# Optimization experiments

Measured on AMD Instinct MI355X. Metric: run time of the kernel, lower is better.

Reference implementation:

```python
import jax, jax.numpy as jnp
import numpy as np

B_SZ, L, H, P, G, N, CS = 2, 2048, 32, 64, 1, 128, 256


def _i8(k, shape):
    return jax.random.randint(k, shape, -127, 128, dtype=jnp.int32).astype(jnp.int8)


def setup_inputs() -> dict:
    key = jax.random.key(0)
    k = jax.random.split(key, 7)
    return {
        "x": _i8(k[0], (B_SZ, L, H, P)),          # quantized int8 activations
        "dt": _i8(k[1], (B_SZ, L, H)),
        "B": _i8(k[2], (B_SZ, L, G, N)),
        "C": _i8(k[3], (B_SZ, L, G, N)),
        "q_A_log": _i8(k[4], (H,)),               # int8 quantized A_log
        "q_D": _i8(k[5], (H,)),                   # int8 quantized D (D_has_hdim=False)
        "dt_bias": jax.random.normal(k[6], (H,), jnp.float32) * 0.1,
        "A_log_scale": jnp.float32(0.02),
        "D_scale": jnp.float32(0.01),
        "dt_scale": jnp.float32(0.03),
        "x_scale": jnp.float32(0.05),
        "B_scale": jnp.float32(0.05),
        "C_scale": jnp.float32(0.05),
    }


def _chunk_scan(x, dt, B, C, q_A_log, q_D, dt_bias,
                A_log_scale, D_scale, dt_scale, x_scale, B_scale, C_scale):
    f32 = jnp.float32
    b, l, h, p = x.shape
    g, n = B.shape[2], B.shape[3]
    cs = CS
    nc = l // cs

    # --- inline dequantization (per-tensor scales, nhead/ndim groups == 0) ---
    xf = x.astype(f32) * x_scale                       # (b, l, h, p)
    dtf = jax.nn.softplus(dt.astype(f32) * dt_scale + dt_bias)   # (b, l, h), dt_limit=(0, inf)
    A = -jnp.exp(q_A_log.astype(f32) * A_log_scale)    # (h,)
    Bf = B.astype(f32) * B_scale                       # (b, l, g, n)
    Cf = C.astype(f32) * C_scale

    # --- chunk the sequence ---
    xc = xf.reshape(b, nc, cs, h, p)
    dtc = dtf.reshape(b, nc, cs, h)
    Bc = Bf.reshape(b, nc, cs, g, n)
    Cc = Cf.reshape(b, nc, cs, g, n)
    rep = h // g
    Bh = jnp.repeat(Bc, rep, axis=3)                   # (b, nc, cs, h, n)
    Ch = jnp.repeat(Cc, rep, axis=3)

    dA = dtc * A                                       # (b, nc, cs, h), <= 0
    cum = jnp.cumsum(dA, axis=2)                       # cumulative log-decay within chunk

    # --- per-chunk states: sum_s exp(cum[-1]-cum[s]) * dt[s] * B[s] (x) x[s] ---
    decay_states = jnp.exp(cum[:, :, -1:, :] - cum)    # (b, nc, cs, h)
    states = jnp.einsum('bzlhn,bzlh,bzlhp->bzhpn', Bh, dtc * decay_states, xc)

    # --- inter-chunk recurrence (sequential scan over chunks) ---
    chunk_decay = jnp.exp(cum[:, :, -1, :])            # (b, nc, h)

    def step(carry, inp):
        s_c, d_c = inp                                 # (b, h, p, n), (b, h)
        new = d_c[:, :, None, None] * carry + s_c
        return new, carry                              # emit state entering this chunk

    states_t = jnp.moveaxis(states, 1, 0)              # (nc, b, h, p, n)
    decay_t = jnp.moveaxis(chunk_decay, 1, 0)          # (nc, b, h)
    final_state, prev_states = jax.lax.scan(
        step, jnp.zeros((b, h, p, n), f32), (states_t, decay_t))
    prev_states = jnp.moveaxis(prev_states, 0, 1)      # (b, nc, h, p, n)

    # --- inter-chunk output: C[l] . state_in * exp(cum[l]) ---
    y_inter = jnp.einsum('bzlhn,bzhpn,bzlh->bzlhp', Ch, prev_states, jnp.exp(cum))

    # --- intra-chunk output: causal (C.B) attention with decay weights ---
    cumT = jnp.moveaxis(cum, 3, 2)                     # (b, nc, h, cs)
    diff = cumT[..., :, None] - cumT[..., None, :]     # (b, nc, h, cs, cs): cum[l]-cum[s]
    mask = jnp.tril(jnp.ones((cs, cs), bool))
    decay_m = jnp.exp(jnp.where(mask, diff, -jnp.inf)) # zero above diagonal, no overflow
    scores = (jnp.einsum('bzlhn,bzshn->bzhls', Ch, Bh)
              * decay_m
              * jnp.moveaxis(dtc, 3, 2)[..., None, :])
    y_intra = jnp.einsum('bzhls,bzshp->bzlhp', scores, xc)

    # --- skip connection D * x (per-head D) ---
    Df = q_D.astype(f32) * D_scale                     # (h,)
    y = (y_intra + y_inter).reshape(b, l, h, p) + xf * Df[None, None, :, None]
    return y


def reference(x, dt, B, C, q_A_log, q_D, dt_bias,
              A_log_scale, D_scale, dt_scale, x_scale, B_scale, C_scale):
    return _chunk_scan(x, dt, B, C, q_A_log, q_D, dt_bias,
                       A_log_scale, D_scale, dt_scale, x_scale, B_scale, C_scale)
```

## Files before the change

kernel.cpp:

```cpp
#include <hip/hip_runtime.h>
#include <math.h>

#define BB 2
#define LSEQ 2048
#define H 32
#define PDIM 64
#define NDIM 128
#define CS 256
#define NC 8

typedef _Float16 half8 __attribute__((ext_vector_type(8)));
typedef float floatx4 __attribute__((ext_vector_type(4)));


__device__ __forceinline__ int dot4i8(int a, int b, int c) {
#if __has_builtin(__builtin_amdgcn_sdot4)
    return __builtin_amdgcn_sdot4(a, b, c, false);
#else
    c += ((a << 24) >> 24) * ((b << 24) >> 24);
    c += ((a << 16) >> 24) * ((b << 16) >> 24);
    c += ((a << 8) >> 24) * ((b << 8) >> 24);
    c += (a >> 24) * (b >> 24);
    return c;
#endif
}

__global__ __launch_bounds__(256) void k1_dtcum(
    const int* __restrict__ dt, const int* __restrict__ qA,
    const float* __restrict__ dt_bias,
    const float* __restrict__ A_scale_p, const float* __restrict__ dt_scale_p,
    float* __restrict__ dtf, float* __restrict__ cum, float* __restrict__ cdecay)
{
    int t = threadIdx.x;
    int h = blockIdx.x & 31;
    int z = (blockIdx.x >> 5) & 7;
    int b = blockIdx.x >> 8;
    int l = z * CS + t;
    float dt_scale = *dt_scale_p;
    float A = -__expf((float)qA[h] * (*A_scale_p));
    float raw = (float)dt[(b * LSEQ + l) * H + h];
    float xin = raw * dt_scale + dt_bias[h];
    float sp = (xin > 20.f) ? xin : log1pf(__expf(xin));
    float dA = sp * A;

    __shared__ float arr[CS];
    arr[t] = dA;
    __syncthreads();
    for (int off = 1; off < CS; off <<= 1) {
        float v = (t >= off) ? arr[t - off] : 0.f;
        __syncthreads();
        arr[t] += v;
        __syncthreads();
    }
    int base = ((b * NC + z) * H + h) * CS;
    dtf[base + t] = sp;
    cum[base + t] = arr[t];
    if (t == CS - 1) cdecay[(b * NC + z) * H + h] = __expf(arr[t]);
}

__global__ __launch_bounds__(256) void k2_cb(
    const int* __restrict__ Bm, const int* __restrict__ Cm,
    const float* __restrict__ Bs_p, const float* __restrict__ Cs_p,
    float* __restrict__ CBt)
{
    __shared__ int Bi[64][33];
    __shared__ int Ci[64][33];
    const int LT[10] = {0,1,1,2,2,2,3,3,3,3};
    const int ST[10] = {0,0,1,0,1,2,0,1,2,3};
    int t = threadIdx.x;
    int tile = blockIdx.x % 10;
    int zz = blockIdx.x / 10;
    int z = zz & 7, b = zz >> 3;
    int bz = b * NC + z;
    int l0 = LT[tile] * 64, s0 = ST[tile] * 64;
    const int* Bp = Bm + (size_t)(b * LSEQ + z * CS + s0) * NDIM;
    const int* Cp = Cm + (size_t)(b * LSEQ + z * CS + l0) * NDIM;
    for (int i = t; i < 64 * 32; i += 256) {
        int r = i >> 5, k = i & 31;
        const int* sb = Bp + r * NDIM + k * 4;
        const int* sc = Cp + r * NDIM + k * 4;
        Bi[r][k] = (sb[0] & 255) | ((sb[1] & 255) << 8) | ((sb[2] & 255) << 16) | ((sb[3] & 255) << 24);
        Ci[r][k] = (sc[0] & 255) | ((sc[1] & 255) << 8) | ((sc[2] & 255) << 16) | ((sc[3] & 255) << 24);
    }
    __syncthreads();
    float cbscale = (*Bs_p) * (*Cs_p);
    int ll = t & 63, lg = t >> 6;
    int acc[16];
#pragma unroll
    for (int i = 0; i < 16; ++i) acc[i] = 0;
    for (int k = 0; k < 32; ++k) {
        int cw = Ci[ll][k];
#pragma unroll
        for (int si = 0; si < 16; ++si)
            acc[si] = dot4i8(cw, Bi[lg * 16 + si][k], acc[si]);
    }
    int l = l0 + ll;
    int l16 = l >> 4, lm = l & 15;
    int sb8 = (s0 + lg * 16) >> 3;
    float* bp = CBt + ((size_t)(bz * 16 + l16) * 32 + sb8) * 128 + lm * 8;
#pragma unroll
    for (int g = 0; g < 2; ++g) {
        floatx4 v0, v1;
#pragma unroll
        for (int i = 0; i < 4; ++i) {
            v0[i] = (float)acc[g * 8 + i] * cbscale;
            v1[i] = (float)acc[g * 8 + 4 + i] * cbscale;
        }
        *(floatx4*)(bp + g * 128) = v0;
        *(floatx4*)(bp + g * 128 + 4) = v1;
    }
}

__global__ __launch_bounds__(256) void kprep(
    const int* __restrict__ Bm, const int* __restrict__ Cm,
    _Float16* __restrict__ Bt16T, _Float16* __restrict__ C16T)
{
    int t = threadIdx.x;
    int slice = blockIdx.x & 15, z = (blockIdx.x >> 4) & 7, b = blockIdx.x >> 7;
    int bz = b * NC + z;
    {
        int lm = t >> 4, n8 = t & 15;
        const int* cp = Cm + (size_t)(b * LSEQ + z * CS + slice * 16 + lm) * NDIM + n8 * 8;
        int4 c0 = *(const int4*)cp;
        int4 c1 = *(const int4*)(cp + 4);
        half8 v;
        v[0] = (_Float16)(float)c0.x; v[1] = (_Float16)(float)c0.y;
        v[2] = (_Float16)(float)c0.z; v[3] = (_Float16)(float)c0.w;
        v[4] = (_Float16)(float)c1.x; v[5] = (_Float16)(float)c1.y;
        v[6] = (_Float16)(float)c1.z; v[7] = (_Float16)(float)c1.w;
        *(half8*)(C16T + ((size_t)(bz * 16 + slice) * 16 + n8) * 128 + lm * 8) = v;
    }
    {
        int nm = t & 15, s8l = t >> 4;
        int n16 = slice & 7, s8 = (slice >> 3) * 16 + s8l;
        const int* bp = Bm + (size_t)(b * LSEQ + z * CS + s8 * 8) * NDIM + n16 * 16 + nm;
        half8 v;
#pragma unroll
        for (int j = 0; j < 8; ++j) v[j] = (_Float16)(float)bp[(size_t)j * NDIM];
        *(half8*)(Bt16T + ((size_t)(bz * 8 + n16) * 32 + s8) * 128 + nm * 8) = v;
    }
}

__global__ __launch_bounds__(256) void k0x(
    const int* __restrict__ xq, const float* __restrict__ dtf, const float* __restrict__ cum,
    const float* __restrict__ xs_p, const float* __restrict__ Bs_p,
    _Float16* __restrict__ xTdtT, _Float16* __restrict__ xTcT)
{
    __shared__ float cA[CS], cB[CS];
    int t = threadIdx.x;
    int h = blockIdx.x & 31, z = (blockIdx.x >> 5) & 7, b = blockIdx.x >> 8;
    int bzh = ((b * NC + z) * H + h);
    int base = bzh * CS;
    float xs = *xs_p, Bs = *Bs_p;
    {
        float d = dtf[base + t], c = cum[base + t], cl = cum[base + CS - 1];
        cA[t] = d * xs;
        cB[t] = d * __expf(cl - c) * xs * Bs;
    }
    __syncthreads();
    int s8 = t & 31, pg = t >> 5;
    const int* xb = xq + ((size_t)(b * LSEQ + z * CS) * H + h) * PDIM + pg * 8;
    half8 va[8], vc[8];
#pragma unroll
    for (int j = 0; j < 8; ++j) {
        int s = s8 * 8 + j;
        const int* xp = xb + (size_t)s * (H * PDIM);
        int4 lo = *(const int4*)xp;
        int4 hi = *(const int4*)(xp + 4);
        float a = cA[s], c = cB[s];
#define CVT(PL, V) { float xv = (float)(V); va[PL][j] = (_Float16)(xv * a); vc[PL][j] = (_Float16)(xv * c); }
        CVT(0, lo.x) CVT(1, lo.y) CVT(2, lo.z) CVT(3, lo.w)
        CVT(4, hi.x) CVT(5, hi.y) CVT(6, hi.z) CVT(7, hi.w)
#undef CVT
    }
    int p16 = pg >> 1;
#pragma unroll
    for (int pl = 0; pl < 8; ++pl) {
        int p = pg * 8 + pl;
        size_t off = ((size_t)(bzh * 4 + p16) * 32 + s8) * 128 + (p & 15) * 8;
        *(half8*)(xTdtT + off) = va[pl];
        *(half8*)(xTcT + off) = vc[pl];
    }
}

__global__ __launch_bounds__(256) void k3m(
    const _Float16* __restrict__ xTcT, const _Float16* __restrict__ Bt16T,
    const float* __restrict__ cum, float* __restrict__ states)
{
    __shared__ float cume[8];
    int t = threadIdx.x;
    int h = blockIdx.x & 31, z = (blockIdx.x >> 5) & 7, b = blockIdx.x >> 8;
    int bz = b * NC + z, bzh = bz * H + h;
    if (t < 8) cume[t] = cum[bzh * CS + t * 32 + 31];
    __syncthreads();
    float cl = cume[7];
    int w = t >> 6, lane = t & 63, m = lane & 15, q = lane >> 4;
    const _Float16* abase = xTcT + ((size_t)(bzh * 4 + w) * 32) * 128 + m * 8;
    const _Float16* bbase = Bt16T + (size_t)(bz * 8) * 32 * 128 + m * 8;
    floatx4 acc[8] = {};
    for (int kk = 0; kk < 8; ++kk) {
        if (cl - cume[kk] < -30.f) continue;
        int s8 = kk * 4 + q;
        half8 a = *(const half8*)(abase + (size_t)s8 * 128);
#pragma unroll
        for (int nt = 0; nt < 8; ++nt) {
            half8 bf = *(const half8*)(bbase + ((size_t)nt * 32 + s8) * 128);
            acc[nt] = __builtin_amdgcn_mfma_f32_16x16x32_f16(a, bf, acc[nt], 0, 0, 0);
        }
    }
    float* sb = states + (size_t)bzh * (PDIM * NDIM);
#pragma unroll
    for (int nt = 0; nt < 8; ++nt)
#pragma unroll
        for (int r = 0; r < 4; ++r)
            sb[(size_t)(w * 16 + q * 4 + r) * NDIM + nt * 16 + m] = acc[nt][r];
}

__global__ __launch_bounds__(256) void k4_scan(
    const float* __restrict__ cdecay, const float* __restrict__ states,
    _Float16* __restrict__ statesHT)
{
    int idx = blockIdx.x * 256 + threadIdx.x;
    int i = idx & 8191, h = (idx >> 13) & 31, b = idx >> 18;
    int p = i >> 7, n = i & 127;
    int toff = ((p >> 4) * 16 + (n >> 3)) * 128 + (p & 15) * 8 + (n & 7);
    float carry = 0.f;
    for (int z = 0; z < NC; ++z) {
        int bzh = (b * NC + z) * H + h;
        float v = states[(size_t)bzh * 8192 + i];
        float d = cdecay[bzh];
        statesHT[(size_t)bzh * 8192 + toff] = (_Float16)(carry * 0.0625f);
        carry = d * carry + v;
    }
}

__global__ __launch_bounds__(256) void k56(
    const int* __restrict__ xq, const int* __restrict__ qD,
    const float* __restrict__ cum, const float* __restrict__ CBt,
    const _Float16* __restrict__ xTdtT, const _Float16* __restrict__ C16T,
    const _Float16* __restrict__ statesHT,
    const float* __restrict__ Cs_p, const float* __restrict__ xs_p, const float* __restrict__ Ds_p,
    float* __restrict__ out)
{
    __shared__ float cumL[CS];
    __shared__ float ep[128][65];
    int t = threadIdx.x;
    int h = blockIdx.x & 31, z = (blockIdx.x >> 5) & 7, b = blockIdx.x >> 8;
    int bz = b * NC + z, bzh = bz * H + h;
    cumL[t] = cum[bzh * CS + t];
    __syncthreads();
    int w = t >> 6, lane = t & 63, m = lane & 15, q = lane >> 4;
    floatx4 acc[4][4] = {};

    const _Float16* shb = statesHT + (size_t)bzh * 8192 + m * 8;
    const _Float16* cbase = C16T + (size_t)bz * 16 * 16 * 128 + m * 8;
    bool interact[4];
#pragma unroll
    for (int j = 0; j < 4; ++j) interact[j] = (cumL[(4 * j + w) * 16] > -80.f);
    for (int kk = 0; kk < 4; ++kk) {
        int n8 = kk * 4 + q;
        half8 bf[4];
#pragma unroll
        for (int pt = 0; pt < 4; ++pt)
            bf[pt] = *(const half8*)(shb + (pt * 16 + n8) * 128);
#pragma unroll
        for (int j = 0; j < 4; ++j) {
            if (!interact[j]) continue;
            half8 ha = *(const half8*)(cbase + ((size_t)(4 * j + w) * 16 + n8) * 128);
#pragma unroll
            for (int pt = 0; pt < 4; ++pt)
                acc[j][pt] = __builtin_amdgcn_mfma_f32_16x16x32_f16(ha, bf[pt], acc[j][pt], 0, 0, 0);
        }
    }
    float Cs16 = (*Cs_p) * 16.0f;
#pragma unroll
    for (int j = 0; j < 4; ++j)
#pragma unroll
        for (int r = 0; r < 4; ++r) {
            float e = __expf(cumL[(4 * j + w) * 16 + q * 4 + r]) * Cs16;
#pragma unroll
            for (int pt = 0; pt < 4; ++pt) acc[j][pt][r] *= e;
        }

    const float* cbtb = CBt + (size_t)bz * 16 * 32 * 128 + m * 8;
    const _Float16* xb = xTdtT + (size_t)bzh * 4 * 32 * 128 + m * 8;
    for (int kk = 0; kk < 8; ++kk) {
        int jmin = (2 * kk - w + 3) >> 2;
        if (jmin < 0) jmin = 0;
        if (jmin > 3) continue;
        int s8 = kk * 4 + q;
        half8 bf[4];
#pragma unroll
        for (int pt = 0; pt < 4; ++pt)
            bf[pt] = *(const half8*)(xb + ((size_t)pt * 32 + s8) * 128);
        float cs_hi = cumL[kk * 32 + 31];
#pragma unroll
        for (int j = 0; j < 4; ++j) {
            if (j < jmin) continue;
            int l16 = 4 * j + w;
            if (cumL[l16 * 16] - cs_hi < -30.f) continue;
            int lA = l16 * 16 + m;
            float cum_l = cumL[lA];
            const float* cp = cbtb + ((size_t)l16 * 32 + s8) * 128;
            floatx4 c0 = *(const floatx4*)cp;
            floatx4 c1 = *(const floatx4*)(cp + 4);
            half8 a;
#pragma unroll
            for (int jj = 0; jj < 8; ++jj) {
                int s = kk * 32 + q * 8 + jj;
                float cb = (jj < 4) ? c0[jj] : c1[jj - 4];
                float wv = cb * __expf(cum_l - cumL[s]);
                a[jj] = (_Float16)((s <= lA) ? wv : 0.f);
            }
#pragma unroll
            for (int pt = 0; pt < 4; ++pt)
                acc[j][pt] = __builtin_amdgcn_mfma_f32_16x16x32_f16(a, bf[pt], acc[j][pt], 0, 0, 0);
        }
    }

    float xsDf = (*xs_p) * ((float)qD[h] * (*Ds_p));
    __syncthreads();
#pragma unroll
    for (int pass = 0; pass < 2; ++pass) {
#pragma unroll
        for (int jj = 0; jj < 2; ++jj) {
            int j = pass * 2 + jj;
            int lbase = (((4 * j + w) * 16) & 127) + q * 4;
#pragma unroll
            for (int r = 0; r < 4; ++r)
#pragma unroll
                for (int pt = 0; pt < 4; ++pt)
                    ep[lbase + r][pt * 16 + m] = acc[j][pt][r];
        }
        __syncthreads();
        int lloc = t >> 1;
        int l = pass * 128 + lloc;
        size_t go = ((size_t)(b * LSEQ + z * CS + l) * H + h) * PDIM + (t & 1) * 32;
        const float* er = &ep[lloc][(t & 1) * 32];
#pragma unroll
        for (int it = 0; it < 8; ++it) {
            int4 xv = *(const int4*)(xq + go + it * 4);
            floatx4 v;
            v[0] = er[it * 4 + 0] + (float)xv.x * xsDf;
            v[1] = er[it * 4 + 1] + (float)xv.y * xsDf;
            v[2] = er[it * 4 + 2] + (float)xv.z * xsDf;
            v[3] = er[it * 4 + 3] + (float)xv.w * xsDf;
            *(floatx4*)(out + go + it * 4) = v;
        }
        __syncthreads();
    }
}

extern "C" void kernel_launch(void* const* d_in, const int* in_sizes, int n_in,
                              void* d_out, int out_size, void* d_ws, size_t ws_size,
                              hipStream_t stream)
{
    const int* xq = (const int*)d_in[0];
    const int* dt = (const int*)d_in[1];
    const int* Bm = (const int*)d_in[2];
    const int* Cm = (const int*)d_in[3];
    const int* qA = (const int*)d_in[4];
    const int* qD = (const int*)d_in[5];
    const float* dt_bias = (const float*)d_in[6];
    const float* A_scale = (const float*)d_in[7];
    const float* D_scale = (const float*)d_in[8];
    const float* dt_scale = (const float*)d_in[9];
    const float* x_scale = (const float*)d_in[10];
    const float* B_scale = (const float*)d_in[11];
    const float* C_scale = (const float*)d_in[12];
    float* out = (float*)d_out;

    char* ws = (char*)d_ws;
    float* dtf          = (float*)(ws);
    float* cum          = (float*)(ws + 524288);
    float* cdecay       = (float*)(ws + 1048576);
    float* CBt          = (float*)(ws + 1052672);
    float* states       = (float*)(ws + 5246976);
    _Float16* xTdtT     = (_Float16*)(ws + 22024192);
    _Float16* xTcT      = (_Float16*)(ws + 38801408);
    _Float16* statesHT  = (_Float16*)(ws + 38801408);
    _Float16* Bt16T     = (_Float16*)(ws + 55578624);
    _Float16* C16T      = (_Float16*)(ws + 56627200);

    k1_dtcum<<<dim3(512), dim3(256), 0, stream>>>(dt, qA, dt_bias, A_scale, dt_scale,
                                                  dtf, cum, cdecay);
    k2_cb<<<dim3(160), dim3(256), 0, stream>>>(Bm, Cm, B_scale, C_scale, CBt);
    kprep<<<dim3(256), dim3(256), 0, stream>>>(Bm, Cm, Bt16T, C16T);
    k0x<<<dim3(512), dim3(256), 0, stream>>>(xq, dtf, cum, x_scale, B_scale, xTdtT, xTcT);
    k3m<<<dim3(512), dim3(256), 0, stream>>>(xTcT, Bt16T, cum, states);
    k4_scan<<<dim3(2048), dim3(256), 0, stream>>>(cdecay, states, statesHT);
    k56<<<dim3(512), dim3(256), 0, stream>>>(xq, qD, cum, CBt, xTdtT, C16T, statesHT,
                                             C_scale, x_scale, D_scale, out);
}
```

Before: 177.0 us.

## Fuse prep kernels, compute chunk states from LDS, compact x to int8

Merges the CB-score and B/C fp16 prep kernels into one launch. A second fused kernel does the dt softplus, the cumulative sum via wavefront shuffles, the x conversion and the state MFMA, keeping the decayed x tile in LDS instead of going through a global buffer. It also writes an int8 copy of x so the final kernel reads a quarter of the bytes for the skip term, and the scan kernel now processes four elements per thread. This cuts launches and global round-trips, at the cost of more LDS and register use in the fused kernel and an extra int8 write.

```diff
diff --git a/kernel.cpp b/kernel.cpp
--- a/kernel.cpp
+++ b/kernel.cpp
@@ -10,6 +10,7 @@
 #define NC 8
 
 typedef _Float16 half8 __attribute__((ext_vector_type(8)));
+typedef _Float16 half4 __attribute__((ext_vector_type(4)));
 typedef float floatx4 __attribute__((ext_vector_type(4)));
 
 
@@ -25,186 +26,174 @@
 #endif
 }
 
-__global__ __launch_bounds__(256) void k1_dtcum(
-    const int* __restrict__ dt, const int* __restrict__ qA,
-    const float* __restrict__ dt_bias,
-    const float* __restrict__ A_scale_p, const float* __restrict__ dt_scale_p,
-    float* __restrict__ dtf, float* __restrict__ cum, float* __restrict__ cdecay)
-{
-    int t = threadIdx.x;
-    int h = blockIdx.x & 31;
-    int z = (blockIdx.x >> 5) & 7;
-    int b = blockIdx.x >> 8;
-    int l = z * CS + t;
-    float dt_scale = *dt_scale_p;
-    float A = -__expf((float)qA[h] * (*A_scale_p));
-    float raw = (float)dt[(b * LSEQ + l) * H + h];
-    float xin = raw * dt_scale + dt_bias[h];
-    float sp = (xin > 20.f) ? xin : log1pf(__expf(xin));
-    float dA = sp * A;
-
-    __shared__ float arr[CS];
-    arr[t] = dA;
-    __syncthreads();
-    for (int off = 1; off < CS; off <<= 1) {
-        float v = (t >= off) ? arr[t - off] : 0.f;
-        __syncthreads();
-        arr[t] += v;
-        __syncthreads();
-    }
-    int base = ((b * NC + z) * H + h) * CS;
-    dtf[base + t] = sp;
-    cum[base + t] = arr[t];
-    if (t == CS - 1) cdecay[(b * NC + z) * H + h] = __expf(arr[t]);
-}
-
-__global__ __launch_bounds__(256) void k2_cb(
+__global__ __launch_bounds__(256) void kA(
     const int* __restrict__ Bm, const int* __restrict__ Cm,
     const float* __restrict__ Bs_p, const float* __restrict__ Cs_p,
-    float* __restrict__ CBt)
+    float* __restrict__ CBt, _Float16* __restrict__ Bt16T, _Float16* __restrict__ C16T)
 {
     __shared__ int Bi[64][33];
     __shared__ int Ci[64][33];
-    const int LT[10] = {0,1,1,2,2,2,3,3,3,3};
-    const int ST[10] = {0,0,1,0,1,2,0,1,2,3};
     int t = threadIdx.x;
-    int tile = blockIdx.x % 10;
-    int zz = blockIdx.x / 10;
+    int r = blockIdx.x % 26;
+    int zz = blockIdx.x / 26;
     int z = zz & 7, b = zz >> 3;
     int bz = b * NC + z;
-    int l0 = LT[tile] * 64, s0 = ST[tile] * 64;
-    const int* Bp = Bm + (size_t)(b * LSEQ + z * CS + s0) * NDIM;
-    const int* Cp = Cm + (size_t)(b * LSEQ + z * CS + l0) * NDIM;
-    for (int i = t; i < 64 * 32; i += 256) {
-        int r = i >> 5, k = i & 31;
-        const int* sb = Bp + r * NDIM + k * 4;
-        const int* sc = Cp + r * NDIM + k * 4;
-        Bi[r][k] = (sb[0] & 255) | ((sb[1] & 255) << 8) | ((sb[2] & 255) << 16) | ((sb[3] & 255) << 24);
-        Ci[r][k] = (sc[0] & 255) | ((sc[1] & 255) << 8) | ((sc[2] & 255) << 16) | ((sc[3] & 255) << 24);
-    }
-    __syncthreads();
-    float cbscale = (*Bs_p) * (*Cs_p);
-    int ll = t & 63, lg = t >> 6;
-    int acc[16];
-#pragma unroll
-    for (int i = 0; i < 16; ++i) acc[i] = 0;
-    for (int k = 0; k < 32; ++k) {
-        int cw = Ci[ll][k];
-#pragma unroll
-        for (int si = 0; si < 16; ++si)
-            acc[si] = dot4i8(cw, Bi[lg * 16 + si][k], acc[si]);
-    }
-    int l = l0 + ll;
-    int l16 = l >> 4, lm = l & 15;
-    int sb8 = (s0 + lg * 16) >> 3;
-    float* bp = CBt + ((size_t)(bz * 16 + l16) * 32 + sb8) * 128 + lm * 8;
-#pragma unroll
-    for (int g = 0; g < 2; ++g) {
-        floatx4 v0, v1;
-#pragma unroll
-        for (int i = 0; i < 4; ++i) {
-            v0[i] = (float)acc[g * 8 + i] * cbscale;
-            v1[i] = (float)acc[g * 8 + 4 + i] * cbscale;
-        }
-        *(floatx4*)(bp + g * 128) = v0;
-        *(floatx4*)(bp + g * 128 + 4) = v1;
-    }
-}
-
-__global__ __launch_bounds__(256) void kprep(
-    const int* __restrict__ Bm, const int* __restrict__ Cm,
-    _Float16* __restrict__ Bt16T, _Float16* __restrict__ C16T)
-{
-    int t = threadIdx.x;
-    int slice = blockIdx.x & 15, z = (blockIdx.x >> 4) & 7, b = blockIdx.x >> 7;
-    int bz = b * NC + z;
-    {
-        int lm = t >> 4, n8 = t & 15;
-        const int* cp = Cm + (size_t)(b * LSEQ + z * CS + slice * 16 + lm) * NDIM + n8 * 8;
-        int4 c0 = *(const int4*)cp;
-        int4 c1 = *(const int4*)(cp + 4);
-        half8 v;
-        v[0] = (_Float16)(float)c0.x; v[1] = (_Float16)(float)c0.y;
-        v[2] = (_Float16)(float)c0.z; v[3] = (_Float16)(float)c0.w;
-        v[4] = (_Float16)(float)c1.x; v[5] = (_Float16)(float)c1.y;
-        v[6] = (_Float16)(float)c1.z; v[7] = (_Float16)(float)c1.w;
-        *(half8*)(C16T + ((size_t)(bz * 16 + slice) * 16 + n8) * 128 + lm * 8) = v;
-    }
-    {
-        int nm = t & 15, s8l = t >> 4;
-        int n16 = slice & 7, s8 = (slice >> 3) * 16 + s8l;
-        const int* bp = Bm + (size_t)(b * LSEQ + z * CS + s8 * 8) * NDIM + n16 * 16 + nm;
-        half8 v;
-#pragma unroll
-        for (int j = 0; j < 8; ++j) v[j] = (_Float16)(float)bp[(size_t)j * NDIM];
-        *(half8*)(Bt16T + ((size_t)(bz * 8 + n16) * 32 + s8) * 128 + nm * 8) = v;
-    }
-}
-
-__global__ __launch_bounds__(256) void k0x(
-    const int* __restrict__ xq, const float* __restrict__ dtf, const float* __restrict__ cum,
-    const float* __restrict__ xs_p, const float* __restrict__ Bs_p,
-    _Float16* __restrict__ xTdtT, _Float16* __restrict__ xTcT)
-{
+    if (r < 10) {
+        const int LT[10] = {0,1,1,2,2,2,3,3,3,3};
+        const int ST[10] = {0,0,1,0,1,2,0,1,2,3};
+        int l0 = LT[r] * 64, s0 = ST[r] * 64;
+        const int* Bp = Bm + (size_t)(b * LSEQ + z * CS + s0) * NDIM;
+        const int* Cp = Cm + (size_t)(b * LSEQ + z * CS + l0) * NDIM;
+        for (int i = t; i < 64 * 32; i += 256) {
+            int rr = i >> 5, k = i & 31;
+            const int* sb = Bp + rr * NDIM + k * 4;
+            const int* sc = Cp + rr * NDIM + k * 4;
+            Bi[rr][k] = (sb[0] & 255) | ((sb[1] & 255) << 8) | ((sb[2] & 255) << 16) | ((sb[3] & 255) << 24);
+            Ci[rr][k] = (sc[0] & 255) | ((sc[1] & 255) << 8) | ((sc[2] & 255) << 16) | ((sc[3] & 255) << 24);
+        }
+        __syncthreads();
+        float cbscale = (*Bs_p) * (*Cs_p);
+        int ll = t & 63, lg = t >> 6;
+        int acc[16];
+#pragma unroll
+        for (int i = 0; i < 16; ++i) acc[i] = 0;
+        for (int k = 0; k < 32; ++k) {
+            int cw = Ci[ll][k];
+#pragma unroll
+            for (int si = 0; si < 16; ++si)
+                acc[si] = dot4i8(cw, Bi[lg * 16 + si][k], acc[si]);
+        }
+        int l = l0 + ll;
+        int l16 = l >> 4, lm = l & 15;
+        int sb8 = (s0 + lg * 16) >> 3;
+        float* bp = CBt + ((size_t)(bz * 16 + l16) * 32 + sb8) * 128 + lm * 8;
+#pragma unroll
+        for (int g = 0; g < 2; ++g) {
+            floatx4 v0, v1;
+#pragma unroll
+            for (int i = 0; i < 4; ++i) {
+                v0[i] = (float)acc[g * 8 + i] * cbscale;
+                v1[i] = (float)acc[g * 8 + 4 + i] * cbscale;
+            }
+            *(floatx4*)(bp + g * 128) = v0;
+            *(floatx4*)(bp + g * 128 + 4) = v1;
+        }
+    } else {
+        int slice = r - 10;
+        {
+            int lm = t >> 4, n8 = t & 15;
+            const int* cp = Cm + (size_t)(b * LSEQ + z * CS + slice * 16 + lm) * NDIM + n8 * 8;
+            int4 c0 = *(const int4*)cp;
+            int4 c1 = *(const int4*)(cp + 4);
+            half8 v;
+            v[0] = (_Float16)(float)c0.x; v[1] = (_Float16)(float)c0.y;
+            v[2] = (_Float16)(float)c0.z; v[3] = (_Float16)(float)c0.w;
+            v[4] = (_Float16)(float)c1.x; v[5] = (_Float16)(float)c1.y;
+            v[6] = (_Float16)(float)c1.z; v[7] = (_Float16)(float)c1.w;
+            *(half8*)(C16T + ((size_t)(bz * 16 + slice) * 16 + n8) * 128 + lm * 8) = v;
+        }
+        {
+            int nm = t & 15, s8l = t >> 4;
+            int n16 = slice & 7, s8 = (slice >> 3) * 16 + s8l;
+            const int* bp = Bm + (size_t)(b * LSEQ + z * CS + s8 * 8) * NDIM + n16 * 16 + nm;
+            half8 v;
+#pragma unroll
+            for (int j = 0; j < 8; ++j) v[j] = (_Float16)(float)bp[(size_t)j * NDIM];
+            *(half8*)(Bt16T + ((size_t)(bz * 8 + n16) * 32 + s8) * 128 + nm * 8) = v;
+        }
+    }
+}
+
+#define XC_PITCH 132
+__global__ __launch_bounds__(256) void k013(
+    const int* __restrict__ dt, const int* __restrict__ qA, const float* __restrict__ dt_bias,
+    const float* __restrict__ A_scale_p, const float* __restrict__ dt_scale_p,
+    const int* __restrict__ xq, const float* __restrict__ xs_p, const float* __restrict__ Bs_p,
+    const _Float16* __restrict__ Bt16T,
+    float* __restrict__ cum, float* __restrict__ cdecay,
+    _Float16* __restrict__ xTdtT, signed char* __restrict__ x8,
+    float* __restrict__ states)
+{
+    __shared__ float cumS[CS];
     __shared__ float cA[CS], cB[CS];
-    int t = threadIdx.x;
-    int h = blockIdx.x & 31, z = (blockIdx.x >> 5) & 7, b = blockIdx.x >> 8;
-    int bzh = ((b * NC + z) * H + h);
-    int base = bzh * CS;
-    float xs = *xs_p, Bs = *Bs_p;
-    {
-        float d = dtf[base + t], c = cum[base + t], cl = cum[base + CS - 1];
-        cA[t] = d * xs;
-        cB[t] = d * __expf(cl - c) * xs * Bs;
-    }
-    __syncthreads();
-    int s8 = t & 31, pg = t >> 5;
-    const int* xb = xq + ((size_t)(b * LSEQ + z * CS) * H + h) * PDIM + pg * 8;
-    half8 va[8], vc[8];
-#pragma unroll
-    for (int j = 0; j < 8; ++j) {
-        int s = s8 * 8 + j;
-        const int* xp = xb + (size_t)s * (H * PDIM);
-        int4 lo = *(const int4*)xp;
-        int4 hi = *(const int4*)(xp + 4);
-        float a = cA[s], c = cB[s];
-#define CVT(PL, V) { float xv = (float)(V); va[PL][j] = (_Float16)(xv * a); vc[PL][j] = (_Float16)(xv * c); }
-        CVT(0, lo.x) CVT(1, lo.y) CVT(2, lo.z) CVT(3, lo.w)
-        CVT(4, hi.x) CVT(5, hi.y) CVT(6, hi.z) CVT(7, hi.w)
-#undef CVT
-    }
-    int p16 = pg >> 1;
-#pragma unroll
-    for (int pl = 0; pl < 8; ++pl) {
-        int p = pg * 8 + pl;
-        size_t off = ((size_t)(bzh * 4 + p16) * 32 + s8) * 128 + (p & 15) * 8;
-        *(half8*)(xTdtT + off) = va[pl];
-        *(half8*)(xTcT + off) = vc[pl];
-    }
-}
-
-__global__ __launch_bounds__(256) void k3m(
-    const _Float16* __restrict__ xTcT, const _Float16* __restrict__ Bt16T,
-    const float* __restrict__ cum, float* __restrict__ states)
-{
-    __shared__ float cume[8];
+    __shared__ float wsum[4];
+    __shared__ _Float16 xcS[4 * 32 * XC_PITCH];
     int t = threadIdx.x;
     int h = blockIdx.x & 31, z = (blockIdx.x >> 5) & 7, b = blockIdx.x >> 8;
     int bz = b * NC + z, bzh = bz * H + h;
-    if (t < 8) cume[t] = cum[bzh * CS + t * 32 + 31];
-    __syncthreads();
-    float cl = cume[7];
-    int w = t >> 6, lane = t & 63, m = lane & 15, q = lane >> 4;
-    const _Float16* abase = xTcT + ((size_t)(bzh * 4 + w) * 32) * 128 + m * 8;
+    int lane6 = t & 63, w = t >> 6;
+
+    float A = -__expf((float)qA[h] * (*A_scale_p));
+    float raw = (float)dt[(size_t)(b * LSEQ + z * CS + t) * H + h];
+    float xin = raw * (*dt_scale_p) + dt_bias[h];
+    float sp = (xin > 20.f) ? xin : log1pf(__expf(xin));
+    float v = sp * A;
+#pragma unroll
+    for (int off = 1; off < 64; off <<= 1) {
+        float u = __shfl_up(v, off, 64);
+        if (lane6 >= off) v += u;
+    }
+    if (lane6 == 63) wsum[w] = v;
+    __syncthreads();
+    float add = 0.f;
+    for (int wv = 0; wv < w; ++wv) add += wsum[wv];
+    float cumv = v + add;
+    float cl = wsum[0] + wsum[1] + wsum[2] + wsum[3];
+    float xs = *xs_p;
+    cum[bzh * CS + t] = cumv;
+    if (t == 0) cdecay[bzh] = __expf(cl);
+    cumS[t] = cumv;
+    cA[t] = sp * xs;
+    cB[t] = sp * __expf(cl - cumv) * xs * (*Bs_p);
+    __syncthreads();
+
+    int s8 = t & 31, pg = t >> 5;
+    const int* xb = xq + ((size_t)(b * LSEQ + z * CS) * H + h) * PDIM + pg * 8;
+    {
+        half8 va[8], vc[8];
+        signed char pk[8][8];
+#pragma unroll
+        for (int j = 0; j < 8; ++j) {
+            int s = s8 * 8 + j;
+            const int* xp = xb + (size_t)s * (H * PDIM);
+            int4 lo = *(const int4*)xp;
+            int4 hi = *(const int4*)(xp + 4);
+            float a = cA[s], c = cB[s];
+#define CVT(PL, V) { float xv = (float)(V); va[PL][j] = (_Float16)(xv * a); vc[PL][j] = (_Float16)(xv * c); pk[j][PL] = (signed char)(V); }
+            CVT(0, lo.x) CVT(1, lo.y) CVT(2, lo.z) CVT(3, lo.w)
+            CVT(4, hi.x) CVT(5, hi.y) CVT(6, hi.z) CVT(7, hi.w)
+#undef CVT
+        }
+        int p16 = pg >> 1;
+#pragma unroll
+        for (int pl = 0; pl < 8; ++pl) {
+            int p = pg * 8 + pl;
+            *(half8*)(xTdtT + ((size_t)(bzh * 4 + p16) * 32 + s8) * 128 + (p & 15) * 8) = va[pl];
+            xcS[(p16 * 32 + s8) * XC_PITCH + (p & 15) * 8 + 0] = vc[pl][0];
+        }
+#pragma unroll
+        for (int pl = 0; pl < 8; ++pl) {
+            int p = pg * 8 + pl;
+            *(half8*)(xcS + (p16 * 32 + s8) * XC_PITCH + (p & 15) * 8) = vc[pl];
+        }
+        signed char* x8b = x8 + ((size_t)(b * LSEQ + z * CS) * H + h) * PDIM + pg * 8;
+#pragma unroll
+        for (int j = 0; j < 8; ++j)
+            *(int2*)(x8b + (size_t)(s8 * 8 + j) * (H * PDIM)) = *(int2*)pk[j];
+    }
+    __syncthreads();
+
+    int m = lane6 & 15, q = lane6 >> 4;
     const _Float16* bbase = Bt16T + (size_t)(bz * 8) * 32 * 128 + m * 8;
+    const _Float16* abase = xcS + (w * 32) * XC_PITCH + m * 8;
     floatx4 acc[8] = {};
     for (int kk = 0; kk < 8; ++kk) {
-        if (cl - cume[kk] < -30.f) continue;
-        int s8 = kk * 4 + q;
-        half8 a = *(const half8*)(abase + (size_t)s8 * 128);
+        if (cl - cumS[kk * 32 + 31] < -30.f) continue;
+        int s8k = kk * 4 + q;
+        half8 a = *(const half8*)(abase + s8k * XC_PITCH);
 #pragma unroll
         for (int nt = 0; nt < 8; ++nt) {
-            half8 bf = *(const half8*)(bbase + ((size_t)nt * 32 + s8) * 128);
+            half8 bf = *(const half8*)(bbase + ((size_t)nt * 32 + s8k) * 128);
             acc[nt] = __builtin_amdgcn_mfma_f32_16x16x32_f16(a, bf, acc[nt], 0, 0, 0);
         }
     }
@@ -212,8 +201,8 @@
 #pragma unroll
     for (int nt = 0; nt < 8; ++nt)
 #pragma unroll
-        for (int r = 0; r < 4; ++r)
-            sb[(size_t)(w * 16 + q * 4 + r) * NDIM + nt * 16 + m] = acc[nt][r];
+        for (int rr = 0; rr < 4; ++rr)
+            sb[(size_t)(w * 16 + q * 4 + rr) * NDIM + nt * 16 + m] = acc[nt][rr];
 }
 
 __global__ __launch_bounds__(256) void k4_scan(
@@ -221,21 +210,25 @@
     _Float16* __restrict__ statesHT)
 {
     int idx = blockIdx.x * 256 + threadIdx.x;
-    int i = idx & 8191, h = (idx >> 13) & 31, b = idx >> 18;
-    int p = i >> 7, n = i & 127;
-    int toff = ((p >> 4) * 16 + (n >> 3)) * 128 + (p & 15) * 8 + (n & 7);
-    float carry = 0.f;
+    int n4 = (idx & 31) * 4, p = (idx >> 5) & 63, h = (idx >> 11) & 31, b = idx >> 16;
+    int soff = p * 128 + n4;
+    int toff = ((p >> 4) * 16 + (n4 >> 3)) * 128 + (p & 15) * 8 + (n4 & 7);
+    floatx4 carry = {};
     for (int z = 0; z < NC; ++z) {
         int bzh = (b * NC + z) * H + h;
-        float v = states[(size_t)bzh * 8192 + i];
+        floatx4 v = *(const floatx4*)(states + (size_t)bzh * 8192 + soff);
         float d = cdecay[bzh];
-        statesHT[(size_t)bzh * 8192 + toff] = (_Float16)(carry * 0.0625f);
-        carry = d * carry + v;
+        half4 o;
+#pragma unroll
+        for (int i = 0; i < 4; ++i) o[i] = (_Float16)(carry[i] * 0.0625f);
+        *(half4*)(statesHT + (size_t)bzh * 8192 + toff) = o;
+#pragma unroll
+        for (int i = 0; i < 4; ++i) carry[i] = d * carry[i] + v[i];
     }
 }
 
 __global__ __launch_bounds__(256) void k56(
-    const int* __restrict__ xq, const int* __restrict__ qD,
+    const signed char* __restrict__ x8, const int* __restrict__ qD,
     const float* __restrict__ cum, const float* __restrict__ CBt,
     const _Float16* __restrict__ xTdtT, const _Float16* __restrict__ C16T,
     const _Float16* __restrict__ statesHT,
@@ -337,14 +330,15 @@
         int l = pass * 128 + lloc;
         size_t go = ((size_t)(b * LSEQ + z * CS + l) * H + h) * PDIM + (t & 1) * 32;
         const float* er = &ep[lloc][(t & 1) * 32];
+        const signed char* xp8 = x8 + go;
 #pragma unroll
         for (int it = 0; it < 8; ++it) {
-            int4 xv = *(const int4*)(xq + go + it * 4);
+            int xw = *(const int*)(xp8 + it * 4);
             floatx4 v;
-            v[0] = er[it * 4 + 0] + (float)xv.x * xsDf;
-            v[1] = er[it * 4 + 1] + (float)xv.y * xsDf;
-            v[2] = er[it * 4 + 2] + (float)xv.z * xsDf;
-            v[3] = er[it * 4 + 3] + (float)xv.w * xsDf;
+            v[0] = er[it * 4 + 0] + (float)((xw << 24) >> 24) * xsDf;
+            v[1] = er[it * 4 + 1] + (float)((xw << 16) >> 24) * xsDf;
+            v[2] = er[it * 4 + 2] + (float)((xw << 8) >> 24) * xsDf;
+            v[3] = er[it * 4 + 3] + (float)(xw >> 24) * xsDf;
             *(floatx4*)(out + go + it * 4) = v;
         }
         __syncthreads();
@@ -371,24 +365,21 @@
     float* out = (float*)d_out;
 
     char* ws = (char*)d_ws;
-    float* dtf          = (float*)(ws);
-    float* cum          = (float*)(ws + 524288);
-    float* cdecay       = (float*)(ws + 1048576);
-    float* CBt          = (float*)(ws + 1052672);
-    float* states       = (float*)(ws + 5246976);
-    _Float16* xTdtT     = (_Float16*)(ws + 22024192);
-    _Float16* xTcT      = (_Float16*)(ws + 38801408);
-    _Float16* statesHT  = (_Float16*)(ws + 38801408);
-    _Float16* Bt16T     = (_Float16*)(ws + 55578624);
-    _Float16* C16T      = (_Float16*)(ws + 56627200);
-
-    k1_dtcum<<<dim3(512), dim3(256), 0, stream>>>(dt, qA, dt_bias, A_scale, dt_scale,
-                                                  dtf, cum, cdecay);
-    k2_cb<<<dim3(160), dim3(256), 0, stream>>>(Bm, Cm, B_scale, C_scale, CBt);
-    kprep<<<dim3(256), dim3(256), 0, stream>>>(Bm, Cm, Bt16T, C16T);
-    k0x<<<dim3(512), dim3(256), 0, stream>>>(xq, dtf, cum, x_scale, B_scale, xTdtT, xTcT);
-    k3m<<<dim3(512), dim3(256), 0, stream>>>(xTcT, Bt16T, cum, states);
-    k4_scan<<<dim3(2048), dim3(256), 0, stream>>>(cdecay, states, statesHT);
-    k56<<<dim3(512), dim3(256), 0, stream>>>(xq, qD, cum, CBt, xTdtT, C16T, statesHT,
+    float* cum          = (float*)(ws);
+    float* cdecay       = (float*)(ws + 524288);
+    float* CBt          = (float*)(ws + 526336);
+    float* states       = (float*)(ws + 4720640);
+    _Float16* xTdtT     = (_Float16*)(ws + 21497856);
+    _Float16* statesHT  = (_Float16*)(ws + 38275072);
+    _Float16* Bt16T     = (_Float16*)(ws + 46663680);
+    _Float16* C16T      = (_Float16*)(ws + 47712256);
+    signed char* x8     = (signed char*)(ws + 48760832);
+
+    kA<<<dim3(416), dim3(256), 0, stream>>>(Bm, Cm, B_scale, C_scale, CBt, Bt16T, C16T);
+    k013<<<dim3(512), dim3(256), 0, stream>>>(dt, qA, dt_bias, A_scale, dt_scale,
+                                              xq, x_scale, B_scale, Bt16T,
+                                              cum, cdecay, xTdtT, x8, states);
+    k4_scan<<<dim3(512), dim3(256), 0, stream>>>(cdecay, states, statesHT);
+    k56<<<dim3(512), dim3(256), 0, stream>>>(x8, qD, cum, CBt, xTdtT, C16T, statesHT,
                                              C_scale, x_scale, D_scale, out);
 }
```

New measurement: 163.5 us. 1.08x faster.
